# Kernel tuning notes

Hardware: AMD Instinct MI355X
Metric: run time of the kernel (lower is better)

The kernel has to match this reference:

```python
import jax, jax.numpy as jnp
import numpy as np

H = 128      # hidden_sizes
E = 128      # embedding_size
V = 100000   # n_words
C = 10       # n_classes
B, S, L = 32, 32, 64
PAD = 0


def _gru_dir(x, w_ih, w_hh, b_ih, b_hh, reverse):
    # x: [N, T, D]; torch GRU cell convention (r, z, n gate order)
    xp = jnp.einsum('ntd,gd->ntg', x, w_ih) + b_ih  # [N, T, 3H]
    if reverse:
        xp = xp[:, ::-1]
    h0 = jnp.zeros((x.shape[0], w_hh.shape[1]), x.dtype)

    def step(h, xt):
        gh = h @ w_hh.T + b_hh
        xr, xz, xn = jnp.split(xt, 3, axis=-1)
        hr, hz, hn = jnp.split(gh, 3, axis=-1)
        r = jax.nn.sigmoid(xr + hr)
        z = jax.nn.sigmoid(xz + hz)
        n = jnp.tanh(xn + r * hn)
        h2 = (1.0 - z) * n + z * h
        return h2, h2

    _, hs = jax.lax.scan(step, h0, jnp.swapaxes(xp, 0, 1))
    hs = jnp.swapaxes(hs, 0, 1)  # [N, T, H]
    if reverse:
        hs = hs[:, ::-1]
    return hs


def _bi_gru(x, pf, pb):
    return jnp.concatenate([_gru_dir(x, *pf, False), _gru_dir(x, *pb, True)], axis=-1)


def _attn_pool(h, W, b, ctx):
    # h: [N, T, 2H] -> pooled [N, 2H]
    u = jnp.tanh(jnp.einsum('ntd,ed->nte', h, W) + b)
    a = jax.nn.softmax(u @ ctx, axis=1)          # [N, T]
    return jnp.einsum('ntd,nt->nd', h, a)


def setup_inputs() -> dict:
    key = jax.random.key(0)
    ks = jax.random.split(key, 24)
    sc = 0.05
    d = {}
    d['X'] = jax.random.randint(ks[0], (B, S, L), 0, V, dtype=jnp.int32)
    d['emb'] = jax.random.normal(ks[1], (V, E), jnp.float32) * sc
    # word-level bi-GRU (input E)
    d['w_ih_f'] = jax.random.normal(ks[2], (3 * H, E), jnp.float32) * sc
    d['w_hh_f'] = jax.random.normal(ks[3], (3 * H, H), jnp.float32) * sc
    d['b_ih_f'] = jnp.zeros((3 * H,), jnp.float32)
    d['b_hh_f'] = jnp.zeros((3 * H,), jnp.float32)
    d['w_ih_b'] = jax.random.normal(ks[4], (3 * H, E), jnp.float32) * sc
    d['w_hh_b'] = jax.random.normal(ks[5], (3 * H, H), jnp.float32) * sc
    d['b_ih_b'] = jnp.zeros((3 * H,), jnp.float32)
    d['b_hh_b'] = jnp.zeros((3 * H,), jnp.float32)
    d['Ww'] = jax.random.normal(ks[6], (2 * H, 2 * H), jnp.float32) * sc
    d['bw'] = jnp.zeros((2 * H,), jnp.float32)
    d['ctx_w'] = jax.random.normal(ks[7], (2 * H,), jnp.float32) * sc
    # sentence-level bi-GRU (input 2H)
    d['s_ih_f'] = jax.random.normal(ks[8], (3 * H, 2 * H), jnp.float32) * sc
    d['s_hh_f'] = jax.random.normal(ks[9], (3 * H, H), jnp.float32) * sc
    d['sb_ih_f'] = jnp.zeros((3 * H,), jnp.float32)
    d['sb_hh_f'] = jnp.zeros((3 * H,), jnp.float32)
    d['s_ih_b'] = jax.random.normal(ks[10], (3 * H, 2 * H), jnp.float32) * sc
    d['s_hh_b'] = jax.random.normal(ks[11], (3 * H, H), jnp.float32) * sc
    d['sb_ih_b'] = jnp.zeros((3 * H,), jnp.float32)
    d['sb_hh_b'] = jnp.zeros((3 * H,), jnp.float32)
    d['Ws'] = jax.random.normal(ks[12], (2 * H, 2 * H), jnp.float32) * sc
    d['bs'] = jnp.zeros((2 * H,), jnp.float32)
    d['ctx_s'] = jax.random.normal(ks[13], (2 * H,), jnp.float32) * sc
    d['Wc'] = jax.random.normal(ks[14], (C, 2 * H), jnp.float32) * sc
    d['bc'] = jnp.zeros((C,), jnp.float32)
    return d


def reference(X, emb, w_ih_f, w_hh_f, b_ih_f, b_hh_f, w_ih_b, w_hh_b, b_ih_b, b_hh_b,
              Ww, bw, ctx_w, s_ih_f, s_hh_f, sb_ih_f, sb_hh_f, s_ih_b, s_hh_b,
              sb_ih_b, sb_hh_b, Ws, bs, ctx_s, Wc, bc):
    emb = emb.at[PAD].set(0.0)               # padding_idx semantics
    words = emb[X.reshape(B * S, L)]          # [B*S, L, E]
    h_w = _bi_gru(words, (w_ih_f, w_hh_f, b_ih_f, b_hh_f),
                  (w_ih_b, w_hh_b, b_ih_b, b_hh_b))  # [B*S, L, 2H]
    sents = _attn_pool(h_w, Ww, bw, ctx_w).reshape(B, S, 2 * H)
    h_s = _bi_gru(sents, (s_ih_f, s_hh_f, sb_ih_f, sb_hh_f),
                  (s_ih_b, s_hh_b, sb_ih_b, sb_hh_b))  # [B, S, 2H]
    doc = _attn_pool(h_s, Ws, bs, ctx_s)      # [B, 2H]
    return doc @ Wc.T + bc                    # [B, C]
```

## Files before the change

### kernel.cpp

```cpp
#include <hip/hip_runtime.h>
#include <hip/hip_bf16.h>
#include <math.h>

#define Bd 32
#define Sd 32
#define Ld 64
#define Ed 128
#define Hd 128
#define MW 65536
#define MS 1024

#define OFF_WIHT_S   0
#define OFF_WFW_W    196608
#define OFF_WFW_S    262144
#define OFF_W6       327680
#define OFF_BIH_W    622592
#define OFF_BIH_S    623360
#define OFF_BHH_W    624128
#define OFF_BHH_S    624896
#define OFF_WFX      625664
#define OFF_HW       723968
#define OFF_SENTS    17763328
#define OFF_XP_S     18025472
#define OFF_HS       18811904
#define OFF_DOC      19078144
#define OFF_WFHH     19086336
#define WS_FLOATS    19184640

typedef __attribute__((ext_vector_type(8))) short sh8;
typedef __attribute__((ext_vector_type(4))) float f32x4;
typedef unsigned short u16;
typedef unsigned int u32;

#define GLD  388
#define XPLD 385
#define HPLD 520

__device__ __forceinline__ void barrier_lds_only() {
    asm volatile("s_waitcnt lgkmcnt(0)\n\ts_barrier" ::: "memory");
}

__device__ __forceinline__ float sigmoidf_(float x) {
    return __fdividef(1.0f, 1.0f + __expf(-x));
}
__device__ __forceinline__ float tanhf_(float x) {
    float t = __expf(-2.0f * fabsf(x));
    float r = __fdividef(1.0f - t, 1.0f + t);
    return copysignf(r, x);
}
__device__ __forceinline__ u16 bf16_hi(float f) {
    u32 x = __float_as_uint(f);
    return (u16)((x + 0x7fffu + ((x >> 16) & 1u)) >> 16);
}
__device__ __forceinline__ float bf16_f(u16 u) { return __uint_as_float(((u32)u) << 16); }
__device__ __forceinline__ void bf16_split(float f, u16& hi, u16& lo) {
    hi = bf16_hi(f);
    lo = bf16_hi(f - bf16_f(hi));
}

__global__ void prep_all(const float* __restrict__ s_ih_f, const float* __restrict__ s_ih_b,
                         const float* __restrict__ w_ih_f, const float* __restrict__ w_ih_b,
                         const float* __restrict__ w_hh_f, const float* __restrict__ w_hh_b,
                         const float* __restrict__ s_hh_f, const float* __restrict__ s_hh_b,
                         const float* __restrict__ b_ih_f, const float* __restrict__ b_ih_b,
                         const float* __restrict__ sb_ih_f, const float* __restrict__ sb_ih_b,
                         const float* __restrict__ b_hh_f, const float* __restrict__ b_hh_b,
                         const float* __restrict__ sb_hh_f, const float* __restrict__ sb_hh_b,
                         const float* __restrict__ Ww, const float* __restrict__ Ws,
                         float* __restrict__ ws)
{
    const int b = blockIdx.x;
    if (b < 1164) {
        int i = b * 256 + threadIdx.x;
        if (i < 294912) {
            int set = i / 49152;
            if (set < 4) return;
            int rem = i % 49152;
            int k4 = rem / 1536, r2 = rem % 1536, g = r2 >> 2, sub = r2 & 3;
            const float* w = (set==4) ? s_hh_f : s_hh_b;
            ws[OFF_W6 + i] = w[g*128 + k4*4 + sub];
            return;
        }
        i -= 294912;
        if (i < 768) { ws[OFF_BIH_W + i] = (i<384) ? b_ih_f[i] : b_ih_b[i-384]; return; }
        i -= 768;
        if (i < 768) { ws[OFF_BIH_S + i] = (i<384) ? sb_ih_f[i] : sb_ih_b[i-384]; return; }
        i -= 768;
        if (i < 768) { ws[OFF_BHH_W + i] = (i<384) ? b_hh_f[i] : b_hh_b[i-384]; return; }
        i -= 768;
        if (i < 768) { ws[OFF_BHH_S + i] = (i<384) ? sb_hh_f[i] : sb_hh_b[i-384]; return; }
        return;
    }
    if (b < 1932) {
        u16* WFo = (u16*)(ws + OFF_WFHH);
        int i = (b - 1164) * 256 + threadIdx.x;
        int within = i % 49152;
        int combo  = i / 49152;
        int half = combo & 1, dir = combo >> 1;
        int nt  = within / 2048;
        int r2  = within % 2048;
        int q   = r2 >> 9;
        int r3  = r2 & 511;
        int l   = r3 >> 3, e = r3 & 7;
        int n = nt*16 + (l & 15);
        int k = q*32 + ((l >> 4) << 3) + e;
        const float* src = dir ? w_hh_b : w_hh_f;
        float v = src[n*128 + k];
        u16 hi = bf16_hi(v);
        WFo[i] = half ? bf16_hi(v - bf16_f(hi)) : hi;
        return;
    }
    if (b < 3724) {
        u16* WFW_W = (u16*)(ws + OFF_WFW_W);
        u16* WFW_S = (u16*)(ws + OFF_WFW_S);
        u16* WFX   = (u16*)(ws + OFF_WFX);
        int i = (b - 1932) * 256 + threadIdx.x;
        if (i < 262144) {
            int which = i / 131072;
            int w = i % 131072;
            int half = w / 65536;
            int r = w % 65536;
            int nt = r / 4096;
            int r2 = r % 4096;
            int q = r2 / 512;
            int l = (r2 % 512) >> 3, e = r2 & 7;
            int n = nt*16 + (l & 15);
            int k = q*32 + ((l >> 4) << 3) + e;
            const float* src = which ? Ws : Ww;
            float v = src[n*256 + k];
            u16 hi = bf16_hi(v);
            u16 o = half ? bf16_hi(v - bf16_f(hi)) : hi;
            (which ? WFW_S : WFW_W)[w] = o;
            return;
        }
        i -= 262144;
        if (i < 196608) {
            int w = i % 98304;
            int dir = i / 98304;
            int half = w / 49152;
            int r = w % 49152;
            int nt = r / 2048;
            int r2 = r % 2048;
            int q = r2 / 512;
            int l = (r2 % 512) >> 3, e = r2 & 7;
            int n = nt*16 + (l & 15);
            int k = q*32 + ((l >> 4) << 3) + e;
            const float* src = dir ? w_ih_b : w_ih_f;
            float v = src[n*128 + k];
            u16 hi = bf16_hi(v);
            WFX[i] = half ? bf16_hi(v - bf16_f(hi)) : hi;
            return;
        }
        return;
    }
    {
        u16* WFIHS = (u16*)(ws + OFF_W6);
        int i = (b - 3724) * 256 + threadIdx.x;
        int dir  = i / 196608;
        int w    = i % 196608;
        int half = w / 98304;
        int r    = w % 98304;
        int nt = r / 4096;
        int r2 = r % 4096;
        int q  = r2 / 512;
        int l  = (r2 % 512) >> 3, e = r2 & 7;
        int n = nt*16 + (l & 15);
        int k = q*32 + ((l >> 4) << 3) + e;
        const float* src = dir ? s_ih_b : s_ih_f;
        float v = src[n*256 + k];
        u16 hi = bf16_hi(v);
        WFIHS[i] = half ? bf16_hi(v - bf16_f(hi)) : hi;
    }
}

__global__ __launch_bounds__(768)
void gru_word_full(const int* __restrict__ X, const float* __restrict__ emb,
                   const u16* __restrict__ WFX, const u16* __restrict__ WFHH,
                   const float* __restrict__ b_ih_f, const float* __restrict__ b_ih_b,
                   const float* __restrict__ b_hh_f, const float* __restrict__ b_hh_b,
                   u16* __restrict__ houtp)
{
    const int bx = blockIdx.x;
    const int dir = bx >> 7;
    const int blk = bx & 127;
    const int seq0 = blk * 8;
    const int tid = threadIdx.x;
    const int lane = tid & 63;
    const int wid = tid >> 6;

    __shared__ float xp_lds[64 * XPLD];
    __shared__ u16 a_pk[8 * 4 * 512];
    __shared__ float G[8 * GLD];
    __shared__ u16 h_pk[4 * HPLD];
    __shared__ int ids_s[8][64];

    const int j = tid & 127;
    const int sg = tid >> 7;
    const bool gthread = tid < 512;
    const float* bih = dir ? b_ih_b : b_ih_f;
    const float* bhh = dir ? b_hh_b : b_hh_f;
    float bhr = 0.f, bhz = 0.f, bhn = 0.f;
    if (gthread) { bhr = bhh[j]; bhz = bhh[128 + j]; bhn = bhh[256 + j]; }

    const u16* WXbase = WFX + (long)dir * 98304;
    const u16* WHbase = WFHH + (long)dir * 98304;
    const int nt0 = wid*2, nt1 = wid*2 + 1;
    const int c0 = nt0*16 + (lane & 15);
    const int c1 = nt1*16 + (lane & 15);
    const int qj = j >> 5, subkj = (j >> 3) & 3, ej = j & 7;

    for (int i = tid; i < 512; i += 768)
        ids_s[i >> 6][i & 63] = X[(long)(seq0 + (i >> 6))*64 + (i & 63)];
    for (int i = tid; i < 4*HPLD; i += 768) h_pk[i] = 0;
    __syncthreads();

    for (int idx = tid; idx < 2048; idx += 768) {
        int cc2 = idx & 1, rm = (idx >> 1) & 7, subk = (idx >> 4) & 3;
        int q = (idx >> 6) & 3, mfs = idx >> 8;
        int t = dir ? 63 - rm : rm;
        int kk = q*32 + subk*8 + cc2*4;
        int id = ids_s[mfs][t];
        float4 v = make_float4(0.f, 0.f, 0.f, 0.f);
        if (id != 0) v = *(const float4*)&emb[(long)id*128 + kk];
        u16 h0,l0,h1,l1,h2,l2,h3,l3;
        bf16_split(v.x,h0,l0); bf16_split(v.y,h1,l1);
        bf16_split(v.z,h2,l2); bf16_split(v.w,h3,l3);
        int lh = subk*16 + rm;
        int base = (mfs*4 + q)*512 + lh*8 + cc2*4;
        uint2 whi = make_uint2((u32)h0 | ((u32)h1 << 16), (u32)h2 | ((u32)h3 << 16));
        uint2 wlo = make_uint2((u32)l0 | ((u32)l1 << 16), (u32)l2 | ((u32)l3 << 16));
        *(uint2*)&a_pk[base]      = whi;
        *(uint2*)&a_pk[base + 64] = wlo;
    }
    __syncthreads();

    float hprev0 = 0.f, hprev1 = 0.f;
    for (int c = 0; c < 8; ++c) {
        asm volatile("" ::: "memory");
        sh8 xh0[4], xl0[4], xh1[4], xl1[4];
#pragma unroll
        for (int q = 0; q < 4; ++q) {
            xh0[q] = *(const sh8*)(WXbase + (nt0*4 + q)*512 + lane*8);
            xl0[q] = *(const sh8*)(WXbase + 49152 + (nt0*4 + q)*512 + lane*8);
            xh1[q] = *(const sh8*)(WXbase + (nt1*4 + q)*512 + lane*8);
            xl1[q] = *(const sh8*)(WXbase + 49152 + (nt1*4 + q)*512 + lane*8);
        }
        const float bv0 = bih[c0], bv1 = bih[c1];
#pragma unroll
        for (int mf = 0; mf < 8; ++mf) {
            f32x4 A0 = (f32x4){0.f,0.f,0.f,0.f};
            f32x4 A1 = (f32x4){0.f,0.f,0.f,0.f};
#pragma unroll
            for (int q = 0; q < 4; ++q) {
                sh8 a = *(const sh8*)&a_pk[(mf*4 + q)*512 + lane*8];
                A0 = __builtin_amdgcn_mfma_f32_16x16x32_bf16(a, xh0[q], A0, 0,0,0);
                A0 = __builtin_amdgcn_mfma_f32_16x16x32_bf16(a, xl0[q], A0, 0,0,0);
                A1 = __builtin_amdgcn_mfma_f32_16x16x32_bf16(a, xh1[q], A1, 0,0,0);
                A1 = __builtin_amdgcn_mfma_f32_16x16x32_bf16(a, xl1[q], A1, 0,0,0);
            }
            float g0[4], g1[4];
#pragma unroll
            for (int r = 0; r < 4; ++r) {
                g0[r] = A0[r] + __shfl_xor(A0[r], 32);
                g1[r] = A1[r] + __shfl_xor(A1[r], 32);
            }
            if ((lane >= 32) == (mf & 1)) {
                int row = mf*8 + ((lane >> 4) & 1)*4;
#pragma unroll
                for (int r = 0; r < 4; ++r) {
                    xp_lds[(row+r)*XPLD + c0] = g0[r] + bv0;
                    xp_lds[(row+r)*XPLD + c1] = g1[r] + bv1;
                }
            }
        }
        barrier_lds_only();
        asm volatile("" ::: "memory");
        sh8 wh0[4], wl0[4], wh1[4], wl1[4];
#pragma unroll
        for (int q = 0; q < 4; ++q) {
            wh0[q] = *(const sh8*)(WHbase + (nt0*4 + q)*512 + lane*8);
            wl0[q] = *(const sh8*)(WHbase + 49152 + (nt0*4 + q)*512 + lane*8);
            wh1[q] = *(const sh8*)(WHbase + (nt1*4 + q)*512 + lane*8);
            wl1[q] = *(const sh8*)(WHbase + 49152 + (nt1*4 + q)*512 + lane*8);
        }
        for (int tt = 0; tt < 8; ++tt) {
            const int ts = c*8 + tt;
            const int t = dir ? 63 - ts : ts;
            float4 sv;
            int s_base = 0;
            const bool sv_ok = !gthread && (c < 7);
            if (sv_ok) {
                const int st = tid - 512;
                const int idx = tt*256 + st;
                int cc2 = idx & 1, rm = (idx >> 1) & 7, subk = (idx >> 4) & 3;
                int q = (idx >> 6) & 3, mfs = idx >> 8;
                int ts2 = (c+1)*8 + rm;
                int t2 = dir ? 63 - ts2 : ts2;
                int kk = q*32 + subk*8 + cc2*4;
                int id = ids_s[mfs][t2];
                sv = make_float4(0.f, 0.f, 0.f, 0.f);
                if (id != 0) sv = *(const float4*)&emb[(long)id*128 + kk];
                int lh = subk*16 + rm;
                s_base = (mfs*4 + q)*512 + lh*8 + cc2*4;
            }
            f32x4 acc0 = (f32x4){0.f,0.f,0.f,0.f};
            f32x4 acc1 = (f32x4){0.f,0.f,0.f,0.f};
#pragma unroll
            for (int q = 0; q < 4; ++q) {
                sh8 hp = *(const sh8*)&h_pk[q*HPLD + lane*8];
                acc0 = __builtin_amdgcn_mfma_f32_16x16x32_bf16(hp, wh0[q], acc0, 0,0,0);
                acc0 = __builtin_amdgcn_mfma_f32_16x16x32_bf16(hp, wl0[q], acc0, 0,0,0);
                acc1 = __builtin_amdgcn_mfma_f32_16x16x32_bf16(hp, wh1[q], acc1, 0,0,0);
                acc1 = __builtin_amdgcn_mfma_f32_16x16x32_bf16(hp, wl1[q], acc1, 0,0,0);
            }
            {
                float sg0[4], sg1[4];
#pragma unroll
                for (int r = 0; r < 4; ++r) {
                    sg0[r] = acc0[r] + __shfl_xor(acc0[r], 32);
                    sg1[r] = acc1[r] + __shfl_xor(acc1[r], 32);
                }
                if (lane < 32) {
                    const int col16 = lane & 15;
                    const int row0  = (lane >> 4) << 2;
#pragma unroll
                    for (int r = 0; r < 4; ++r) {
                        G[(row0+r)*GLD + nt0*16 + col16] = sg0[r];
                        G[(row0+r)*GLD + nt1*16 + col16] = sg1[r];
                    }
                }
            }
            barrier_lds_only();
            if (gthread) {
#pragma unroll
                for (int si = 0; si < 2; ++si) {
                    const int s = sg + si*4;
                    float gr  = G[s*GLD + j]       + bhr;
                    float gz  = G[s*GLD + 128 + j] + bhz;
                    float gnh = G[s*GLD + 256 + j] + bhn;
                    const float* xrow = &xp_lds[(s*8 + tt)*XPLD];
                    float r  = sigmoidf_(xrow[j] + gr);
                    float z  = sigmoidf_(xrow[128 + j] + gz);
                    float nv = tanhf_(xrow[256 + j] + r * gnh);
                    float hold = si ? hprev1 : hprev0;
                    float hnew = (1.f - z) * nv + z * hold;
                    if (si) hprev1 = hnew; else hprev0 = hnew;
                    u16 hh, hl; bf16_split(hnew, hh, hl);
                    u16 ohh = (u16)__shfl_xor((int)hh, 1);
                    u16 ohl = (u16)__shfl_xor((int)hl, 1);
                    const long tbase = ((long)(seq0 + s)*64 + t)*512 + dir*128;
                    if ((j & 1) == 0) {
                        u32 w = (u32)hh | ((u32)ohh << 16);
                        *(u32*)&h_pk[qj*HPLD + (subkj*16 + s)*8 + ej] = w;
                        *(u32*)&houtp[tbase + j] = w;
                    } else {
                        u32 w = (u32)ohl | ((u32)hl << 16);
                        *(u32*)&h_pk[qj*HPLD + (subkj*16 + s + 8)*8 + (ej - 1)] = w;
                        *(u32*)&houtp[tbase + 256 + (j - 1)] = w;
                    }
                }
            } else if (sv_ok) {
                u16 h0,l0,h1,l1,h2,l2,h3,l3;
                bf16_split(sv.x,h0,l0); bf16_split(sv.y,h1,l1);
                bf16_split(sv.z,h2,l2); bf16_split(sv.w,h3,l3);
                uint2 whi = make_uint2((u32)h0 | ((u32)h1 << 16), (u32)h2 | ((u32)h3 << 16));
                uint2 wlo = make_uint2((u32)l0 | ((u32)l1 << 16), (u32)l2 | ((u32)l3 << 16));
                *(uint2*)&a_pk[s_base]      = whi;
                *(uint2*)&a_pk[s_base + 64] = wlo;
            }
            barrier_lds_only();
        }
    }
}

template<int T, bool PACKED, bool CLS>
__global__ __launch_bounds__(1024)
void attn_fused(const float* __restrict__ A, const u16* __restrict__ WF,
                const float* __restrict__ bias, const float* __restrict__ ctx,
                float* __restrict__ outp,
                const float* __restrict__ Wc, const float* __restrict__ bc)
{
    __shared__ u16 a_pk[8][8][512];
    __shared__ float pscore[8][8][17];
    __shared__ float aw[64];
    __shared__ float red[4][256];
    __shared__ float docv[2][256];
    const int tid = threadIdx.x;
    const int lane = tid & 63;
    const int wid = tid >> 6;
    const int m0 = blockIdx.x * 64;

    sh8 bh[8], bl[8];
#pragma unroll
    for (int q = 0; q < 8; ++q) {
        bh[q] = *(const sh8*)(WF + (wid*8 + q)*512 + lane*8);
        bl[q] = *(const sh8*)(WF + 65536 + (wid*8 + q)*512 + lane*8);
    }
    const int colg = wid*16 + (lane & 15);
    const float bwv = bias[colg];
    const float cxv = ctx[colg];

    if (PACKED) {
        const u32* src32 = (const u32*)A + (long)blockIdx.x * 16384;
        u32* dst = (u32*)a_pk;
        for (int idx4 = tid; idx4 < 4096; idx4 += 1024) {
            int idx = idx4 << 2;
            int mf = idx >> 11, q = (idx >> 8) & 7, l = (idx >> 2) & 63;
            int row16 = l & 15, hilo = row16 >> 3, rm = row16 & 7;
            int t = mf*8 + rm;
            int kb2 = q*16 + (l >> 4)*4;
            *(uint4*)&dst[idx] = *(const uint4*)&src32[(t*2 + hilo)*128 + kb2];
        }
    } else {
        for (int idx = tid; idx < 8192; idx += 1024) {
            int row = idx >> 7;
            int k   = (idx & 127) << 1;
            float2 v = *(const float2*)&A[(long)(m0 + row)*256 + k];
            u16 h0,l0,h1,l1; bf16_split(v.x,h0,l0); bf16_split(v.y,h1,l1);
            int mf = row >> 3, rm = row & 7;
            int q = k >> 5;
            int lh = (((k & 31) >> 3) << 4) | rm;
            int e = k & 7;
            *(u32*)&a_pk[mf][q][lh*8 + e]     = (u32)h0 | ((u32)h1 << 16);
            *(u32*)&a_pk[mf][q][(lh+8)*8 + e] = (u32)l0 | ((u32)l1 << 16);
        }
    }
    __syncthreads();

#pragma unroll
    for (int mf = 0; mf < 8; ++mf) {
        f32x4 acc = (f32x4){0.f,0.f,0.f,0.f};
#pragma unroll
        for (int q = 0; q < 8; ++q) {
            sh8 a = *(const sh8*)&a_pk[mf][q][lane*8];
            acc = __builtin_amdgcn_mfma_f32_16x16x32_bf16(a, bh[q], acc, 0,0,0);
            acc = __builtin_amdgcn_mfma_f32_16x16x32_bf16(a, bl[q], acc, 0,0,0);
        }
        float g[4];
#pragma unroll
        for (int r = 0; r < 4; ++r) g[r] = acc[r] + __shfl_xor(acc[r], 32);
        if ((lane >= 32) == (mf & 1)) {
            float p[4];
#pragma unroll
            for (int r = 0; r < 4; ++r) p[r] = tanhf_(g[r] + bwv) * cxv;
#pragma unroll
            for (int r = 0; r < 4; ++r) {
                p[r] += __shfl_xor(p[r], 1);
                p[r] += __shfl_xor(p[r], 2);
                p[r] += __shfl_xor(p[r], 4);
                p[r] += __shfl_xor(p[r], 8);
            }
            if ((lane & 15) == 0) {
#pragma unroll
                for (int r = 0; r < 4; ++r)
                    pscore[mf][((lane >> 4) & 1)*4 + r][wid] = p[r];
            }
        }
    }
    __syncthreads();

    if (tid < 64) {
        float sc = 0.f;
#pragma unroll
        for (int w = 0; w < 16; ++w) sc += pscore[tid >> 3][tid & 7][w];
        float mx = sc;
#pragma unroll
        for (int m = 1; m < T; m <<= 1) mx = fmaxf(mx, __shfl_xor(mx, m));
        float e = __expf(sc - mx);
        float den = e;
#pragma unroll
        for (int m = 1; m < T; m <<= 1) den += __shfl_xor(den, m);
        aw[tid] = __fdividef(e, den);
    }
    __syncthreads();

    if (tid < 512) {
        const int dp = (tid & 127) << 1;
        const int tg = tid >> 7;
        const int q = dp >> 5, lhb = ((dp & 31) >> 3) << 4, e = dp & 7;
        float acc0 = 0.f, acc1 = 0.f;
#pragma unroll
        for (int i = 0; i < 16; ++i) {
            int t = tg*16 + i;
            int mf = t >> 3, rm = t & 7;
            const u16* base = &a_pk[mf][q][(lhb | rm)*8 + e];
            u32 hh = *(const u32*)base;
            u32 ll = *(const u32*)(base + 64);
            float h0 = bf16_f((u16)hh) + bf16_f((u16)ll);
            float h1 = bf16_f((u16)(hh >> 16)) + bf16_f((u16)(ll >> 16));
            float w = aw[t];
            acc0 = fmaf(w, h0, acc0);
            acc1 = fmaf(w, h1, acc1);
        }
        red[tg][dp] = acc0; red[tg][dp + 1] = acc1;
    }
    __syncthreads();
    if (T == 64) {
        if (tid < 256)
            outp[(long)blockIdx.x*256 + tid] = red[0][tid] + red[1][tid] + red[2][tid] + red[3][tid];
    } else if (!CLS) {
        if (tid < 512) {
            int sent = tid >> 8, dd = tid & 255;
            outp[((long)blockIdx.x*2 + sent)*256 + dd] = red[sent*2][dd] + red[sent*2 + 1][dd];
        }
    } else {
        if (tid < 512) {
            int sent = tid >> 8, dd = tid & 255;
            docv[sent][dd] = red[sent*2][dd] + red[sent*2 + 1][dd];
        }
        __syncthreads();
        if (tid < 20) {
            int s = tid / 10, c = tid % 10;
            float acc = bc[c];
            const float4* wp = (const float4*)&Wc[c*256];
            const float4* dv = (const float4*)&docv[s][0];
#pragma unroll 8
            for (int d = 0; d < 64; ++d) {
                float4 a = dv[d], w = wp[d];
                acc = fmaf(a.x, w.x, fmaf(a.y, w.y, fmaf(a.z, w.z, fmaf(a.w, w.w, acc))));
            }
            outp[(blockIdx.x*2 + s)*10 + c] = acc;
        }
    }
}

__global__ __launch_bounds__(512)
void gru_sent(const float* __restrict__ sents, const u16* __restrict__ WFIHS,
              const float* __restrict__ bih_s, const float4* __restrict__ whh4,
              const float* __restrict__ bhh, float* __restrict__ hout)
{
    const int bx = blockIdx.x;
    const int dir = bx >> 5;
    const int doc = bx & 31;
    const int tid = threadIdx.x;
    const int lane = tid & 63;
    const int wid = tid >> 6;

    __shared__ float xp_lds[32 * XPLD];
    __shared__ u16 a_pk[4 * 8 * 512];
    __shared__ float h_lds[128];

    for (int i = tid; i < 128; i += 512) h_lds[i] = 0.f;

    for (int idx = tid; idx < 2048; idx += 512) {
        int cc2 = idx & 1, rm = (idx >> 1) & 7, subk = (idx >> 4) & 3;
        int q = (idx >> 6) & 7, mf = (idx >> 9) & 3;
        int t = mf*8 + rm;
        int kk = q*32 + subk*8 + cc2*4;
        float4 v = *(const float4*)&sents[(long)(doc*32 + t)*256 + kk];
        u16 h0,l0,h1,l1,h2,l2,h3,l3;
        bf16_split(v.x,h0,l0); bf16_split(v.y,h1,l1);
        bf16_split(v.z,h2,l2); bf16_split(v.w,h3,l3);
        int lh = subk*16 + rm;
        int base = (mf*8 + q)*512 + lh*8 + cc2*4;
        uint2 whi = make_uint2((u32)h0 | ((u32)h1 << 16), (u32)h2 | ((u32)h3 << 16));
        uint2 wlo = make_uint2((u32)l0 | ((u32)l1 << 16), (u32)l2 | ((u32)l3 << 16));
        *(uint2*)&a_pk[base]      = whi;
        *(uint2*)&a_pk[base + 64] = wlo;
    }
    barrier_lds_only();

    const u16* WFbase = WFIHS + (long)dir * 196608;
#pragma unroll 1
    for (int ni = 0; ni < 3; ++ni) {
        const int nt = wid + ni*8;
        sh8 wh[8], wl[8];
#pragma unroll
        for (int q = 0; q < 8; ++q) {
            wh[q] = *(const sh8*)(WFbase + (nt*8 + q)*512 + lane*8);
            wl[q] = *(const sh8*)(WFbase + 98304 + (nt*8 + q)*512 + lane*8);
        }
        const int col16 = lane & 15;
        const float bv = bih_s[dir*384 + nt*16 + col16];
        f32x4 A0 = (f32x4){0.f,0.f,0.f,0.f};
        f32x4 A1 = (f32x4){0.f,0.f,0.f,0.f};
        f32x4 A2 = (f32x4){0.f,0.f,0.f,0.f};
        f32x4 A3 = (f32x4){0.f,0.f,0.f,0.f};
#pragma unroll
        for (int q = 0; q < 8; ++q) {
            sh8 a0 = *(const sh8*)&a_pk[(0*8 + q)*512 + lane*8];
            sh8 a1 = *(const sh8*)&a_pk[(1*8 + q)*512 + lane*8];
            sh8 a2 = *(const sh8*)&a_pk[(2*8 + q)*512 + lane*8];
            sh8 a3 = *(const sh8*)&a_pk[(3*8 + q)*512 + lane*8];
            A0 = __builtin_amdgcn_mfma_f32_16x16x32_bf16(a0, wh[q], A0, 0,0,0);
            A0 = __builtin_amdgcn_mfma_f32_16x16x32_bf16(a0, wl[q], A0, 0,0,0);
            A1 = __builtin_amdgcn_mfma_f32_16x16x32_bf16(a1, wh[q], A1, 0,0,0);
            A1 = __builtin_amdgcn_mfma_f32_16x16x32_bf16(a1, wl[q], A1, 0,0,0);
            A2 = __builtin_amdgcn_mfma_f32_16x16x32_bf16(a2, wh[q], A2, 0,0,0);
            A2 = __builtin_amdgcn_mfma_f32_16x16x32_bf16(a2, wl[q], A2, 0,0,0);
            A3 = __builtin_amdgcn_mfma_f32_16x16x32_bf16(a3, wh[q], A3, 0,0,0);
            A3 = __builtin_amdgcn_mfma_f32_16x16x32_bf16(a3, wl[q], A3, 0,0,0);
        }
#pragma unroll
        for (int mf = 0; mf < 4; ++mf) {
            f32x4 A = (mf==0) ? A0 : (mf==1) ? A1 : (mf==2) ? A2 : A3;
            float g[4];
#pragma unroll
            for (int r = 0; r < 4; ++r) g[r] = A[r] + __shfl_xor(A[r], 32);
            if ((lane >= 32) == (mf & 1)) {
                int row = mf*8 + ((lane >> 4) & 1)*4;
#pragma unroll
                for (int r = 0; r < 4; ++r)
                    xp_lds[(row+r)*XPLD + nt*16 + col16] = g[r] + bv;
            }
        }
    }
    barrier_lds_only();
    asm volatile("" ::: "memory");

    const int kq = tid & 3;
    const int j  = tid >> 2;
    const float4* W = whh4 + (long)dir * 12288;
    const float bhr = bhh[dir*384 + j];
    const float bhz = bhh[dir*384 + 128 + j];
    const float bhn = bhh[dir*384 + 256 + j];
    float4 w0r[8], w1r[8], w2r[8];
#pragma unroll
    for (int ii = 0; ii < 8; ++ii) {
        const int k4 = kq + (ii << 2);
        w0r[ii] = W[k4*384 + j];
        w1r[ii] = W[k4*384 + 128 + j];
        w2r[ii] = W[k4*384 + 256 + j];
    }

    for (int ts = 0; ts < 32; ++ts) {
        const int t = dir ? (31 - ts) : ts;
        float a0 = 0.f, a1 = 0.f, a2 = 0.f;
#pragma unroll
        for (int ii = 0; ii < 8; ++ii) {
            const int k4 = kq + (ii << 2);
            float4 w0 = w0r[ii];
            float4 w1 = w1r[ii];
            float4 w2 = w2r[ii];
            float4 h4 = *(const float4*)&h_lds[k4 << 2];
            a0 = fmaf(w0.x,h4.x, fmaf(w0.y,h4.y, fmaf(w0.z,h4.z, fmaf(w0.w,h4.w, a0))));
            a1 = fmaf(w1.x,h4.x, fmaf(w1.y,h4.y, fmaf(w1.z,h4.z, fmaf(w1.w,h4.w, a1))));
            a2 = fmaf(w2.x,h4.x, fmaf(w2.y,h4.y, fmaf(w2.z,h4.z, fmaf(w2.w,h4.w, a2))));
        }
        a0 += __shfl_xor(a0, 1); a0 += __shfl_xor(a0, 2);
        a1 += __shfl_xor(a1, 1); a1 += __shfl_xor(a1, 2);
        a2 += __shfl_xor(a2, 1); a2 += __shfl_xor(a2, 2);
        __syncthreads();
        if (kq == 0) {
            const float* xr = &xp_lds[t*XPLD];
            float r = sigmoidf_(xr[j]       + a0 + bhr);
            float z = sigmoidf_(xr[128 + j] + a1 + bhz);
            float nv = tanhf_(xr[256 + j] + r * (a2 + bhn));
            float hold = h_lds[j];
            float hnew = (1.f - z) * nv + z * hold;
            h_lds[j] = hnew;
            hout[((long)(doc*32 + t))*256 + dir*128 + j] = hnew;
        }
        __syncthreads();
    }
}

extern "C" void kernel_launch(void* const* d_in, const int* in_sizes, int n_in,
                              void* d_out, int out_size, void* d_ws, size_t ws_size,
                              hipStream_t stream) {
    const int*   X       = (const int*)  d_in[0];
    const float* emb     = (const float*)d_in[1];
    const float* w_ih_f  = (const float*)d_in[2];
    const float* w_hh_f  = (const float*)d_in[3];
    const float* b_ih_f  = (const float*)d_in[4];
    const float* b_hh_f  = (const float*)d_in[5];
    const float* w_ih_b  = (const float*)d_in[6];
    const float* w_hh_b  = (const float*)d_in[7];
    const float* b_ih_b  = (const float*)d_in[8];
    const float* b_hh_b  = (const float*)d_in[9];
    const float* Ww      = (const float*)d_in[10];
    const float* bw      = (const float*)d_in[11];
    const float* ctx_w   = (const float*)d_in[12];
    const float* s_ih_f  = (const float*)d_in[13];
    const float* s_hh_f  = (const float*)d_in[14];
    const float* sb_ih_f = (const float*)d_in[15];
    const float* sb_hh_f = (const float*)d_in[16];
    const float* s_ih_b  = (const float*)d_in[17];
    const float* s_hh_b  = (const float*)d_in[18];
    const float* sb_ih_b = (const float*)d_in[19];
    const float* sb_hh_b = (const float*)d_in[20];
    const float* Ws      = (const float*)d_in[21];
    const float* bs      = (const float*)d_in[22];
    const float* ctx_s   = (const float*)d_in[23];
    const float* Wc      = (const float*)d_in[24];
    const float* bc      = (const float*)d_in[25];
    float* ws  = (float*)d_ws;
    float* out = (float*)d_out;

    if (ws_size < (size_t)WS_FLOATS * 4) return;

    prep_all<<<5260, 256, 0, stream>>>(s_ih_f, s_ih_b, w_ih_f, w_ih_b,
                                       w_hh_f, w_hh_b, s_hh_f, s_hh_b,
                                       b_ih_f, b_ih_b, sb_ih_f, sb_ih_b,
                                       b_hh_f, b_hh_b, sb_hh_f, sb_hh_b,
                                       Ww, Ws, ws);

    gru_word_full<<<256, 768, 0, stream>>>(
        X, emb, (const u16*)(ws + OFF_WFX), (const u16*)(ws + OFF_WFHH),
        b_ih_f, b_ih_b, b_hh_f, b_hh_b, (u16*)(ws + OFF_HW));

    attn_fused<64, true, false><<<1024, 1024, 0, stream>>>(
        ws + OFF_HW, (const u16*)(ws + OFF_WFW_W), bw, ctx_w, ws + OFF_SENTS,
        nullptr, nullptr);

    gru_sent<<<64, 512, 0, stream>>>(
        ws + OFF_SENTS, (const u16*)(ws + OFF_W6), ws + OFF_BIH_S,
        (const float4*)(ws + OFF_W6) + 4*12288, ws + OFF_BHH_S, ws + OFF_HS);

    attn_fused<32, false, true><<<16, 1024, 0, stream>>>(
        ws + OFF_HS, (const u16*)(ws + OFF_WFW_S), bs, ctx_s, out, Wc, bc);
}
```

Before: 307.3 us.

## Fuse sentence GRU both directions with sentence attention and classifier

After: 345.4 us. +12.4%, slower.

```diff
diff --git a/kernel.cpp b/kernel.cpp
--- a/kernel.cpp
+++ b/kernel.cpp
@@ -10,7 +10,6 @@
 #define MW 65536
 #define MS 1024
 
-#define OFF_WIHT_S   0
 #define OFF_WFW_W    196608
 #define OFF_WFW_S    262144
 #define OFF_W6       327680
@@ -21,9 +20,6 @@
 #define OFF_WFX      625664
 #define OFF_HW       723968
 #define OFF_SENTS    17763328
-#define OFF_XP_S     18025472
-#define OFF_HS       18811904
-#define OFF_DOC      19078144
 #define OFF_WFHH     19086336
 #define WS_FLOATS    19184640
 
@@ -373,22 +369,20 @@
     }
 }
 
-template<int T, bool PACKED, bool CLS>
 __global__ __launch_bounds__(1024)
-void attn_fused(const float* __restrict__ A, const u16* __restrict__ WF,
-                const float* __restrict__ bias, const float* __restrict__ ctx,
-                float* __restrict__ outp,
-                const float* __restrict__ Wc, const float* __restrict__ bc)
+void attn_word(const float* __restrict__ A, const u16* __restrict__ WF,
+               const float* __restrict__ bias, const float* __restrict__ ctx,
+               float* __restrict__ outp)
 {
     __shared__ u16 a_pk[8][8][512];
     __shared__ float pscore[8][8][17];
     __shared__ float aw[64];
     __shared__ float red[4][256];
-    __shared__ float docv[2][256];
     const int tid = threadIdx.x;
     const int lane = tid & 63;
     const int wid = tid >> 6;
-    const int m0 = blockIdx.x * 64;
+    const int i = blockIdx.x;
+    const int s = ((i >> 3) & 15) * 64 + (i & 7) * 8 + (i >> 7);
 
     sh8 bh[8], bl[8];
 #pragma unroll
@@ -400,8 +394,8 @@
     const float bwv = bias[colg];
     const float cxv = ctx[colg];
 
-    if (PACKED) {
-        const u32* src32 = (const u32*)A + (long)blockIdx.x * 16384;
+    {
+        const u32* src32 = (const u32*)A + (long)s * 16384;
         u32* dst = (u32*)a_pk;
         for (int idx4 = tid; idx4 < 4096; idx4 += 1024) {
             int idx = idx4 << 2;
@@ -411,19 +405,6 @@
             int kb2 = q*16 + (l >> 4)*4;
             *(uint4*)&dst[idx] = *(const uint4*)&src32[(t*2 + hilo)*128 + kb2];
         }
-    } else {
-        for (int idx = tid; idx < 8192; idx += 1024) {
-            int row = idx >> 7;
-            int k   = (idx & 127) << 1;
-            float2 v = *(const float2*)&A[(long)(m0 + row)*256 + k];
-            u16 h0,l0,h1,l1; bf16_split(v.x,h0,l0); bf16_split(v.y,h1,l1);
-            int mf = row >> 3, rm = row & 7;
-            int q = k >> 5;
-            int lh = (((k & 31) >> 3) << 4) | rm;
-            int e = k & 7;
-            *(u32*)&a_pk[mf][q][lh*8 + e]     = (u32)h0 | ((u32)h1 << 16);
-            *(u32*)&a_pk[mf][q][(lh+8)*8 + e] = (u32)l0 | ((u32)l1 << 16);
-        }
     }
     __syncthreads();
 
@@ -465,11 +446,11 @@
         for (int w = 0; w < 16; ++w) sc += pscore[tid >> 3][tid & 7][w];
         float mx = sc;
 #pragma unroll
-        for (int m = 1; m < T; m <<= 1) mx = fmaxf(mx, __shfl_xor(mx, m));
+        for (int m = 1; m < 64; m <<= 1) mx = fmaxf(mx, __shfl_xor(mx, m));
         float e = __expf(sc - mx);
         float den = e;
 #pragma unroll
-        for (int m = 1; m < T; m <<= 1) den += __shfl_xor(den, m);
+        for (int m = 1; m < 64; m <<= 1) den += __shfl_xor(den, m);
         aw[tid] = __fdividef(e, den);
     }
     __syncthreads();
@@ -480,8 +461,8 @@
         const int q = dp >> 5, lhb = ((dp & 31) >> 3) << 4, e = dp & 7;
         float acc0 = 0.f, acc1 = 0.f;
 #pragma unroll
-        for (int i = 0; i < 16; ++i) {
-            int t = tg*16 + i;
+        for (int ii = 0; ii < 16; ++ii) {
+            int t = tg*16 + ii;
             int mf = t >> 3, rm = t & 7;
             const u16* base = &a_pk[mf][q][(lhb | rm)*8 + e];
             u32 hh = *(const u32*)base;
@@ -495,54 +476,35 @@
         red[tg][dp] = acc0; red[tg][dp + 1] = acc1;
     }
     __syncthreads();
-    if (T == 64) {
-        if (tid < 256)
-            outp[(long)blockIdx.x*256 + tid] = red[0][tid] + red[1][tid] + red[2][tid] + red[3][tid];
-    } else if (!CLS) {
-        if (tid < 512) {
-            int sent = tid >> 8, dd = tid & 255;
-            outp[((long)blockIdx.x*2 + sent)*256 + dd] = red[sent*2][dd] + red[sent*2 + 1][dd];
-        }
-    } else {
-        if (tid < 512) {
-            int sent = tid >> 8, dd = tid & 255;
-            docv[sent][dd] = red[sent*2][dd] + red[sent*2 + 1][dd];
-        }
-        __syncthreads();
-        if (tid < 20) {
-            int s = tid / 10, c = tid % 10;
-            float acc = bc[c];
-            const float4* wp = (const float4*)&Wc[c*256];
-            const float4* dv = (const float4*)&docv[s][0];
-#pragma unroll 8
-            for (int d = 0; d < 64; ++d) {
-                float4 a = dv[d], w = wp[d];
-                acc = fmaf(a.x, w.x, fmaf(a.y, w.y, fmaf(a.z, w.z, fmaf(a.w, w.w, acc))));
-            }
-            outp[(blockIdx.x*2 + s)*10 + c] = acc;
-        }
-    }
-}
-
-__global__ __launch_bounds__(512)
-void gru_sent(const float* __restrict__ sents, const u16* __restrict__ WFIHS,
-              const float* __restrict__ bih_s, const float4* __restrict__ whh4,
-              const float* __restrict__ bhh, float* __restrict__ hout)
+    if (tid < 256)
+        outp[(long)s*256 + tid] = red[0][tid] + red[1][tid] + red[2][tid] + red[3][tid];
+}
+
+__global__ __launch_bounds__(1024)
+void gru_sent_attn(const float* __restrict__ sents, const u16* __restrict__ WFIHS,
+                   const float* __restrict__ bih_s, const float4* __restrict__ whh4,
+                   const float* __restrict__ bhh,
+                   const u16* __restrict__ WFA, const float* __restrict__ bs,
+                   const float* __restrict__ ctx_s,
+                   const float* __restrict__ Wc, const float* __restrict__ bc,
+                   float* __restrict__ outp)
 {
-    const int bx = blockIdx.x;
-    const int dir = bx >> 5;
-    const int doc = bx & 31;
+    const int doc = blockIdx.x;
     const int tid = threadIdx.x;
     const int lane = tid & 63;
     const int wid = tid >> 6;
 
-    __shared__ float xp_lds[32 * XPLD];
-    __shared__ u16 a_pk[4 * 8 * 512];
-    __shared__ float h_lds[128];
-
-    for (int i = tid; i < 128; i += 512) h_lds[i] = 0.f;
-
-    for (int idx = tid; idx < 2048; idx += 512) {
+    __shared__ float xp_lds[2][32 * XPLD];
+    __shared__ u16 apk[4 * 8 * 512];
+    __shared__ float h_lds[2][128];
+    __shared__ float pscore[4][8][17];
+    __shared__ float aw[32];
+    __shared__ float red[4][256];
+    __shared__ float docv[256];
+
+    if (tid < 256) h_lds[tid >> 7][tid & 127] = 0.f;
+
+    for (int idx = tid; idx < 2048; idx += 1024) {
         int cc2 = idx & 1, rm = (idx >> 1) & 7, subk = (idx >> 4) & 3;
         int q = (idx >> 6) & 7, mf = (idx >> 9) & 3;
         int t = mf*8 + rm;
@@ -555,103 +517,223 @@
         int base = (mf*8 + q)*512 + lh*8 + cc2*4;
         uint2 whi = make_uint2((u32)h0 | ((u32)h1 << 16), (u32)h2 | ((u32)h3 << 16));
         uint2 wlo = make_uint2((u32)l0 | ((u32)l1 << 16), (u32)l2 | ((u32)l3 << 16));
-        *(uint2*)&a_pk[base]      = whi;
-        *(uint2*)&a_pk[base + 64] = wlo;
+        *(uint2*)&apk[base]      = whi;
+        *(uint2*)&apk[base + 64] = wlo;
     }
     barrier_lds_only();
 
-    const u16* WFbase = WFIHS + (long)dir * 196608;
+    {
+        const int pdir = wid >> 3;
+        const int lw = wid & 7;
+        const u16* WFbase = WFIHS + (long)pdir * 196608;
 #pragma unroll 1
-    for (int ni = 0; ni < 3; ++ni) {
-        const int nt = wid + ni*8;
-        sh8 wh[8], wl[8];
-#pragma unroll
-        for (int q = 0; q < 8; ++q) {
-            wh[q] = *(const sh8*)(WFbase + (nt*8 + q)*512 + lane*8);
-            wl[q] = *(const sh8*)(WFbase + 98304 + (nt*8 + q)*512 + lane*8);
-        }
-        const int col16 = lane & 15;
-        const float bv = bih_s[dir*384 + nt*16 + col16];
-        f32x4 A0 = (f32x4){0.f,0.f,0.f,0.f};
-        f32x4 A1 = (f32x4){0.f,0.f,0.f,0.f};
-        f32x4 A2 = (f32x4){0.f,0.f,0.f,0.f};
-        f32x4 A3 = (f32x4){0.f,0.f,0.f,0.f};
-#pragma unroll
-        for (int q = 0; q < 8; ++q) {
-            sh8 a0 = *(const sh8*)&a_pk[(0*8 + q)*512 + lane*8];
-            sh8 a1 = *(const sh8*)&a_pk[(1*8 + q)*512 + lane*8];
-            sh8 a2 = *(const sh8*)&a_pk[(2*8 + q)*512 + lane*8];
-            sh8 a3 = *(const sh8*)&a_pk[(3*8 + q)*512 + lane*8];
-            A0 = __builtin_amdgcn_mfma_f32_16x16x32_bf16(a0, wh[q], A0, 0,0,0);
-            A0 = __builtin_amdgcn_mfma_f32_16x16x32_bf16(a0, wl[q], A0, 0,0,0);
-            A1 = __builtin_amdgcn_mfma_f32_16x16x32_bf16(a1, wh[q], A1, 0,0,0);
-            A1 = __builtin_amdgcn_mfma_f32_16x16x32_bf16(a1, wl[q], A1, 0,0,0);
-            A2 = __builtin_amdgcn_mfma_f32_16x16x32_bf16(a2, wh[q], A2, 0,0,0);
-            A2 = __builtin_amdgcn_mfma_f32_16x16x32_bf16(a2, wl[q], A2, 0,0,0);
-            A3 = __builtin_amdgcn_mfma_f32_16x16x32_bf16(a3, wh[q], A3, 0,0,0);
-            A3 = __builtin_amdgcn_mfma_f32_16x16x32_bf16(a3, wl[q], A3, 0,0,0);
-        }
-#pragma unroll
-        for (int mf = 0; mf < 4; ++mf) {
-            f32x4 A = (mf==0) ? A0 : (mf==1) ? A1 : (mf==2) ? A2 : A3;
-            float g[4];
-#pragma unroll
-            for (int r = 0; r < 4; ++r) g[r] = A[r] + __shfl_xor(A[r], 32);
-            if ((lane >= 32) == (mf & 1)) {
-                int row = mf*8 + ((lane >> 4) & 1)*4;
-#pragma unroll
-                for (int r = 0; r < 4; ++r)
-                    xp_lds[(row+r)*XPLD + nt*16 + col16] = g[r] + bv;
+        for (int ni = 0; ni < 3; ++ni) {
+            const int nt = lw + ni*8;
+            sh8 wh[8], wl[8];
+#pragma unroll
+            for (int q = 0; q < 8; ++q) {
+                wh[q] = *(const sh8*)(WFbase + (nt*8 + q)*512 + lane*8);
+                wl[q] = *(const sh8*)(WFbase + 98304 + (nt*8 + q)*512 + lane*8);
+            }
+            const int col16 = lane & 15;
+            const float bv = bih_s[pdir*384 + nt*16 + col16];
+            f32x4 A0 = (f32x4){0.f,0.f,0.f,0.f};
+            f32x4 A1 = (f32x4){0.f,0.f,0.f,0.f};
+            f32x4 A2 = (f32x4){0.f,0.f,0.f,0.f};
+            f32x4 A3 = (f32x4){0.f,0.f,0.f,0.f};
+#pragma unroll
+            for (int q = 0; q < 8; ++q) {
+                sh8 a0 = *(const sh8*)&apk[(0*8 + q)*512 + lane*8];
+                sh8 a1 = *(const sh8*)&apk[(1*8 + q)*512 + lane*8];
+                sh8 a2 = *(const sh8*)&apk[(2*8 + q)*512 + lane*8];
+                sh8 a3 = *(const sh8*)&apk[(3*8 + q)*512 + lane*8];
+                A0 = __builtin_amdgcn_mfma_f32_16x16x32_bf16(a0, wh[q], A0, 0,0,0);
+                A0 = __builtin_amdgcn_mfma_f32_16x16x32_bf16(a0, wl[q], A0, 0,0,0);
+                A1 = __builtin_amdgcn_mfma_f32_16x16x32_bf16(a1, wh[q], A1, 0,0,0);
+                A1 = __builtin_amdgcn_mfma_f32_16x16x32_bf16(a1, wl[q], A1, 0,0,0);
+                A2 = __builtin_amdgcn_mfma_f32_16x16x32_bf16(a2, wh[q], A2, 0,0,0);
+                A2 = __builtin_amdgcn_mfma_f32_16x16x32_bf16(a2, wl[q], A2, 0,0,0);
+                A3 = __builtin_amdgcn_mfma_f32_16x16x32_bf16(a3, wh[q], A3, 0,0,0);
+                A3 = __builtin_amdgcn_mfma_f32_16x16x32_bf16(a3, wl[q], A3, 0,0,0);
+            }
+#pragma unroll
+            for (int mf = 0; mf < 4; ++mf) {
+                f32x4 A = (mf==0) ? A0 : (mf==1) ? A1 : (mf==2) ? A2 : A3;
+                float g[4];
+#pragma unroll
+                for (int r = 0; r < 4; ++r) g[r] = A[r] + __shfl_xor(A[r], 32);
+                if ((lane >= 32) == (mf & 1)) {
+                    int row = mf*8 + ((lane >> 4) & 1)*4;
+#pragma unroll
+                    for (int r = 0; r < 4; ++r)
+                        xp_lds[pdir][(row+r)*XPLD + nt*16 + col16] = g[r] + bv;
+                }
             }
         }
     }
     barrier_lds_only();
     asm volatile("" ::: "memory");
 
-    const int kq = tid & 3;
-    const int j  = tid >> 2;
-    const float4* W = whh4 + (long)dir * 12288;
-    const float bhr = bhh[dir*384 + j];
-    const float bhz = bhh[dir*384 + 128 + j];
-    const float bhn = bhh[dir*384 + 256 + j];
-    float4 w0r[8], w1r[8], w2r[8];
-#pragma unroll
-    for (int ii = 0; ii < 8; ++ii) {
-        const int k4 = kq + (ii << 2);
-        w0r[ii] = W[k4*384 + j];
-        w1r[ii] = W[k4*384 + 128 + j];
-        w2r[ii] = W[k4*384 + 256 + j];
-    }
-
-    for (int ts = 0; ts < 32; ++ts) {
-        const int t = dir ? (31 - ts) : ts;
-        float a0 = 0.f, a1 = 0.f, a2 = 0.f;
-#pragma unroll
-        for (int ii = 0; ii < 8; ++ii) {
+    {
+        const int d3 = tid >> 9;
+        const int dtid = tid & 511;
+        const int kq = dtid & 3;
+        const int j  = dtid >> 2;
+        const float4* W = whh4 + (long)d3 * 12288;
+        const float bhr = bhh[d3*384 + j];
+        const float bhz = bhh[d3*384 + 128 + j];
+        const float bhn = bhh[d3*384 + 256 + j];
+        float4 w0r[4], w1r[4], w2r[4];
+#pragma unroll
+        for (int ii = 0; ii < 4; ++ii) {
             const int k4 = kq + (ii << 2);
-            float4 w0 = w0r[ii];
-            float4 w1 = w1r[ii];
-            float4 w2 = w2r[ii];
-            float4 h4 = *(const float4*)&h_lds[k4 << 2];
-            a0 = fmaf(w0.x,h4.x, fmaf(w0.y,h4.y, fmaf(w0.z,h4.z, fmaf(w0.w,h4.w, a0))));
-            a1 = fmaf(w1.x,h4.x, fmaf(w1.y,h4.y, fmaf(w1.z,h4.z, fmaf(w1.w,h4.w, a1))));
-            a2 = fmaf(w2.x,h4.x, fmaf(w2.y,h4.y, fmaf(w2.z,h4.z, fmaf(w2.w,h4.w, a2))));
-        }
-        a0 += __shfl_xor(a0, 1); a0 += __shfl_xor(a0, 2);
-        a1 += __shfl_xor(a1, 1); a1 += __shfl_xor(a1, 2);
-        a2 += __shfl_xor(a2, 1); a2 += __shfl_xor(a2, 2);
+            w0r[ii] = W[k4*384 + j];
+            w1r[ii] = W[k4*384 + 128 + j];
+            w2r[ii] = W[k4*384 + 256 + j];
+        }
+        const int ka = d3*128 + j;
+        const int qa = ka >> 5, subka = (ka >> 3) & 3, ea = ka & 7;
+
+        for (int ts = 0; ts < 32; ++ts) {
+            const int t = d3 ? (31 - ts) : ts;
+            float a0 = 0.f, a1 = 0.f, a2 = 0.f;
+#pragma unroll
+            for (int ii = 0; ii < 4; ++ii) {
+                const int k4 = kq + (ii << 2);
+                float4 w0 = w0r[ii], w1 = w1r[ii], w2 = w2r[ii];
+                float4 h4 = *(const float4*)&h_lds[d3][k4 << 2];
+                a0 = fmaf(w0.x,h4.x, fmaf(w0.y,h4.y, fmaf(w0.z,h4.z, fmaf(w0.w,h4.w, a0))));
+                a1 = fmaf(w1.x,h4.x, fmaf(w1.y,h4.y, fmaf(w1.z,h4.z, fmaf(w1.w,h4.w, a1))));
+                a2 = fmaf(w2.x,h4.x, fmaf(w2.y,h4.y, fmaf(w2.z,h4.z, fmaf(w2.w,h4.w, a2))));
+            }
+#pragma unroll
+            for (int ii = 4; ii < 8; ++ii) {
+                const int k4 = kq + (ii << 2);
+                float4 w0 = W[k4*384 + j];
+                float4 w1 = W[k4*384 + 128 + j];
+                float4 w2 = W[k4*384 + 256 + j];
+                float4 h4 = *(const float4*)&h_lds[d3][k4 << 2];
+                a0 = fmaf(w0.x,h4.x, fmaf(w0.y,h4.y, fmaf(w0.z,h4.z, fmaf(w0.w,h4.w, a0))));
+                a1 = fmaf(w1.x,h4.x, fmaf(w1.y,h4.y, fmaf(w1.z,h4.z, fmaf(w1.w,h4.w, a1))));
+                a2 = fmaf(w2.x,h4.x, fmaf(w2.y,h4.y, fmaf(w2.z,h4.z, fmaf(w2.w,h4.w, a2))));
+            }
+            a0 += __shfl_xor(a0, 1); a0 += __shfl_xor(a0, 2);
+            a1 += __shfl_xor(a1, 1); a1 += __shfl_xor(a1, 2);
+            a2 += __shfl_xor(a2, 1); a2 += __shfl_xor(a2, 2);
+            __syncthreads();
+            if (kq == 0) {
+                const float* xr = &xp_lds[d3][t*XPLD];
+                float r = sigmoidf_(xr[j]       + a0 + bhr);
+                float z = sigmoidf_(xr[128 + j] + a1 + bhz);
+                float nv = tanhf_(xr[256 + j] + r * (a2 + bhn));
+                float hold = h_lds[d3][j];
+                float hnew = (1.f - z) * nv + z * hold;
+                h_lds[d3][j] = hnew;
+                int mf = t >> 3, rm = t & 7;
+                int lh = subka*16 + rm;
+                u16 hh, hl; bf16_split(hnew, hh, hl);
+                apk[(mf*8 + qa)*512 + lh*8 + ea]       = hh;
+                apk[(mf*8 + qa)*512 + (lh+8)*8 + ea]   = hl;
+            }
+            __syncthreads();
+        }
+    }
+
+    {
+        sh8 bh[8], bl[8];
+#pragma unroll
+        for (int q = 0; q < 8; ++q) {
+            bh[q] = *(const sh8*)(WFA + (wid*8 + q)*512 + lane*8);
+            bl[q] = *(const sh8*)(WFA + 65536 + (wid*8 + q)*512 + lane*8);
+        }
+        const int colg = wid*16 + (lane & 15);
+        const float bwv = bs[colg];
+        const float cxv = ctx_s[colg];
+
+#pragma unroll
+        for (int mf = 0; mf < 4; ++mf) {
+            f32x4 acc = (f32x4){0.f,0.f,0.f,0.f};
+#pragma unroll
+            for (int q = 0; q < 8; ++q) {
+                sh8 a = *(const sh8*)&apk[(mf*8 + q)*512 + lane*8];
+                acc = __builtin_amdgcn_mfma_f32_16x16x32_bf16(a, bh[q], acc, 0,0,0);
+                acc = __builtin_amdgcn_mfma_f32_16x16x32_bf16(a, bl[q], acc, 0,0,0);
+            }
+            float g[4];
+#pragma unroll
+            for (int r = 0; r < 4; ++r) g[r] = acc[r] + __shfl_xor(acc[r], 32);
+            if ((lane >= 32) == (mf & 1)) {
+                float p[4];
+#pragma unroll
+                for (int r = 0; r < 4; ++r) p[r] = tanhf_(g[r] + bwv) * cxv;
+#pragma unroll
+                for (int r = 0; r < 4; ++r) {
+                    p[r] += __shfl_xor(p[r], 1);
+                    p[r] += __shfl_xor(p[r], 2);
+                    p[r] += __shfl_xor(p[r], 4);
+                    p[r] += __shfl_xor(p[r], 8);
+                }
+                if ((lane & 15) == 0) {
+#pragma unroll
+                    for (int r = 0; r < 4; ++r)
+                        pscore[mf][((lane >> 4) & 1)*4 + r][wid] = p[r];
+                }
+            }
+        }
         __syncthreads();
-        if (kq == 0) {
-            const float* xr = &xp_lds[t*XPLD];
-            float r = sigmoidf_(xr[j]       + a0 + bhr);
-            float z = sigmoidf_(xr[128 + j] + a1 + bhz);
-            float nv = tanhf_(xr[256 + j] + r * (a2 + bhn));
-            float hold = h_lds[j];
-            float hnew = (1.f - z) * nv + z * hold;
-            h_lds[j] = hnew;
-            hout[((long)(doc*32 + t))*256 + dir*128 + j] = hnew;
+
+        if (tid < 32) {
+            float sc = 0.f;
+#pragma unroll
+            for (int w = 0; w < 16; ++w) sc += pscore[tid >> 3][tid & 7][w];
+            float mx = sc;
+#pragma unroll
+            for (int m = 1; m < 32; m <<= 1) mx = fmaxf(mx, __shfl_xor(mx, m));
+            float e = __expf(sc - mx);
+            float den = e;
+#pragma unroll
+            for (int m = 1; m < 32; m <<= 1) den += __shfl_xor(den, m);
+            aw[tid] = __fdividef(e, den);
         }
         __syncthreads();
+
+        if (tid < 512) {
+            const int dp = (tid & 127) << 1;
+            const int tg = tid >> 7;
+            const int q = dp >> 5, lhb = ((dp & 31) >> 3) << 4, e = dp & 7;
+            float acc0 = 0.f, acc1 = 0.f;
+#pragma unroll
+            for (int ii = 0; ii < 8; ++ii) {
+                int t = tg*8 + ii;
+                int mf = t >> 3, rm = t & 7;
+                const u16* base = &apk[(mf*8 + q)*512 + (lhb | rm)*8 + e];
+                u32 hh = *(const u32*)base;
+                u32 ll = *(const u32*)(base + 64);
+                float h0 = bf16_f((u16)hh) + bf16_f((u16)ll);
+                float h1 = bf16_f((u16)(hh >> 16)) + bf16_f((u16)(ll >> 16));
+                float w = aw[t];
+                acc0 = fmaf(w, h0, acc0);
+                acc1 = fmaf(w, h1, acc1);
+            }
+            red[tg][dp] = acc0; red[tg][dp + 1] = acc1;
+        }
+        __syncthreads();
+        if (tid < 256)
+            docv[tid] = red[0][tid] + red[1][tid] + red[2][tid] + red[3][tid];
+        __syncthreads();
+
+        if (tid < 10) {
+            const int c = tid;
+            float acc = bc[c];
+            const float4* wp = (const float4*)&Wc[c*256];
+            const float4* dv = (const float4*)&docv[0];
+#pragma unroll 8
+            for (int d = 0; d < 64; ++d) {
+                float4 a = dv[d], w = wp[d];
+                acc = fmaf(a.x, w.x, fmaf(a.y, w.y, fmaf(a.z, w.z, fmaf(a.w, w.w, acc))));
+            }
+            outp[doc*10 + c] = acc;
+        }
     }
 }
 
@@ -699,14 +781,11 @@
         X, emb, (const u16*)(ws + OFF_WFX), (const u16*)(ws + OFF_WFHH),
         b_ih_f, b_ih_b, b_hh_f, b_hh_b, (u16*)(ws + OFF_HW));
 
-    attn_fused<64, true, false><<<1024, 1024, 0, stream>>>(
-        ws + OFF_HW, (const u16*)(ws + OFF_WFW_W), bw, ctx_w, ws + OFF_SENTS,
-        nullptr, nullptr);
-
-    gru_sent<<<64, 512, 0, stream>>>(
+    attn_word<<<1024, 1024, 0, stream>>>(
+        ws + OFF_HW, (const u16*)(ws + OFF_WFW_W), bw, ctx_w, ws + OFF_SENTS);
+
+    gru_sent_attn<<<32, 1024, 0, stream>>>(
         ws + OFF_SENTS, (const u16*)(ws + OFF_W6), ws + OFF_BIH_S,
-        (const float4*)(ws + OFF_W6) + 4*12288, ws + OFF_BHH_S, ws + OFF_HS);
-
-    attn_fused<32, false, true><<<16, 1024, 0, stream>>>(
-        ws + OFF_HS, (const u16*)(ws + OFF_WFW_S), bs, ctx_s, out, Wc, bc);
-}
+        (const float4*)(ws + OFF_W6) + 4*12288, ws + OFF_BHH_S,
+        (const u16*)(ws + OFF_WFW_S), bs, ctx_s, Wc, bc, out);
+}
```
